# Performance work log

Hardware: AMD Instinct MI355X
Metric: run time of the kernel (lower is better)

Reference implementation:

```python
import jax, jax.numpy as jnp
import numpy as np

N_NODES = 50000
N_EDGES = 800000
IN_FEATS = 96
H_FEATS = 256
N_HOPS = 3
N_NIE = N_HOPS + 1  # hops 0..3
NDIM_FC = N_NIE * H_FEATS


def setup_inputs() -> dict:
    key = jax.random.key(0)
    ks = jax.random.split(key, 8)
    edge_index = jax.random.randint(ks[0], (2, N_EDGES), 0, N_NODES, dtype=jnp.int64)
    features = jax.random.normal(ks[1], (N_NODES, IN_FEATS), dtype=jnp.float32)
    # per-hop MLP params: Linear(in_feats, h_feats) for each of n_nie hops
    s_in = 1.0 / np.sqrt(IN_FEATS)
    Ws = jax.random.uniform(ks[2], (N_NIE, IN_FEATS, H_FEATS), jnp.float32, -s_in, s_in)
    bs = jax.random.uniform(ks[3], (N_NIE, H_FEATS), jnp.float32, -s_in, s_in)
    # fusion: Linear(ndim_fc, h_feats)
    s_fc = 1.0 / np.sqrt(NDIM_FC)
    Wf = jax.random.uniform(ks[4], (NDIM_FC, H_FEATS), jnp.float32, -s_fc, s_fc)
    bf = jax.random.uniform(ks[5], (H_FEATS,), jnp.float32, -s_fc, s_fc)
    return {"edge_index": edge_index, "features": features, "Ws": Ws, "bs": bs, "Wf": Wf, "bf": bf}


def _build_norm_adj(edge_index):
    """set_diag (remove existing diag, add unit self-loops) + symmetric D^-1/2 A D^-1/2.
    Returns (rows, cols, edge_w) COO of the normalized adjacency."""
    row, col = edge_index[0].astype(jnp.int32), edge_index[1].astype(jnp.int32)
    loop = jnp.arange(N_NODES, dtype=jnp.int32)
    rows = jnp.concatenate([row, loop])
    cols = jnp.concatenate([col, loop])
    # zero out any pre-existing diagonal entries, self-loops get weight 1 (set_diag semantics)
    w = jnp.concatenate([(row != col).astype(jnp.float32), jnp.ones((N_NODES,), jnp.float32)])
    deg = jax.ops.segment_sum(w, rows, num_segments=N_NODES)
    dinv = jnp.where(deg > 0, jax.lax.rsqrt(deg), 0.0)
    edge_w = dinv[rows] * w * dinv[cols]
    return rows, cols, edge_w


def _spmm(rows, cols, edge_w, x):
    # out[r] = sum_e w_e * x[cols[e]] for edges with rows[e]==r
    return jax.ops.segment_sum(edge_w[:, None] * x[cols], rows, num_segments=N_NODES)


def reference(edge_index, features, Ws, bs, Wf, bf):
    rows, cols, edge_w = _build_norm_adj(edge_index)
    # row-normalize features (F.normalize dim=1)
    x = features / jnp.maximum(jnp.linalg.norm(features, axis=1, keepdims=True), 1e-12)
    nei_feats = [x]
    h = x
    for _ in range(N_HOPS):
        h = _spmm(rows, cols, edge_w, h)
        nei_feats.append(h)
    # per-hop MLP (dropout p=0 -> identity; norm=None -> identity) then ReLU
    ns = [jax.nn.relu(nei_feats[i] @ Ws[i] + bs[i]) for i in range(N_NIE)]
    cat = jnp.concatenate(ns, axis=1)  # [N, ndim_fc]
    out = jax.nn.relu(cat @ Wf + bf)   # [N, h_feats]
    return out
```

## Files before the change

kernel.cpp:

```cpp
#include <hip/hip_runtime.h>

#define N_NODES 50000
#define N_EDGES 800000
#define IN_F 96
#define H_F 256
#define N_NIE 4
#define SCAN_NB 196
#define BM 64
#define NBLK 782
#define LDA1 104

typedef float f32x4 __attribute__((ext_vector_type(4)));
typedef short s16x8 __attribute__((ext_vector_type(8)));
typedef unsigned short ushort;

__device__ __forceinline__ ushort bf16_rne(float f) {
    unsigned u = __float_as_uint(f);
    u += 0x7fffu + ((u >> 16) & 1u);
    return (ushort)(u >> 16);
}
__device__ __forceinline__ float bf16_f(ushort h) {
    return __uint_as_float(((unsigned)h) << 16);
}

__global__ __launch_bounds__(256) void k_count(const int* __restrict__ rows,
                                               const int* __restrict__ cols,
                                               int* __restrict__ cnt) {
    int i = blockIdx.x * 256 + threadIdx.x;
    if (i >= N_EDGES / 2) return;
    int2 r2 = ((const int2*)rows)[i];
    int2 c2 = ((const int2*)cols)[i];
    if (r2.x != c2.x) atomicAdd(&cnt[r2.x], 1);
    if (r2.y != c2.y) atomicAdd(&cnt[r2.y], 1);
}

__global__ __launch_bounds__(256) void k_scan1(const int* __restrict__ cnt,
                                               int* __restrict__ rowptr,
                                               int* __restrict__ bsum) {
    __shared__ int s[256];
    int t = threadIdx.x, e = blockIdx.x * 256 + t;
    int v = (e < N_NODES) ? cnt[e] : 0;
    s[t] = v;
    __syncthreads();
    #pragma unroll
    for (int off = 1; off < 256; off <<= 1) {
        int nv = (t >= off) ? s[t - off] : 0;
        __syncthreads();
        s[t] += nv;
        __syncthreads();
    }
    if (e < N_NODES) rowptr[e] = s[t] - v;
    if (t == 255) bsum[blockIdx.x] = s[255];
}

__global__ __launch_bounds__(256) void k_scan2(int* __restrict__ bsum,
                                               int* __restrict__ boff,
                                               int* __restrict__ rowptr) {
    __shared__ int s[256];
    int t = threadIdx.x;
    int v = (t < SCAN_NB) ? bsum[t] : 0;
    s[t] = v;
    __syncthreads();
    #pragma unroll
    for (int off = 1; off < 256; off <<= 1) {
        int nv = (t >= off) ? s[t - off] : 0;
        __syncthreads();
        s[t] += nv;
        __syncthreads();
    }
    if (t < SCAN_NB) boff[t] = s[t] - v;
    if (t == 255) rowptr[N_NODES] = s[255];
}

__global__ __launch_bounds__(256) void k_scan3(const int* __restrict__ boff,
                                               const int* __restrict__ cnt,
                                               int* __restrict__ rowptr,
                                               int* __restrict__ cursor,
                                               float* __restrict__ dinv) {
    int e = blockIdx.x * 256 + threadIdx.x;
    if (e >= N_NODES) return;
    int r = rowptr[e] + boff[blockIdx.x];
    rowptr[e] = r;
    cursor[e] = r;
    dinv[e] = rsqrtf((float)cnt[e] + 1.0f);
}

__global__ __launch_bounds__(256) void k_scatter(const int* __restrict__ rows,
                                                 const int* __restrict__ cols,
                                                 const float* __restrict__ dinv,
                                                 int* __restrict__ cursor,
                                                 int2* __restrict__ cw) {
    int e = blockIdx.x * 256 + threadIdx.x;
    if (e >= N_EDGES) return;
    int r = rows[e], c = cols[e];
    if (r == c) return;
    int p = atomicAdd(&cursor[r], 1);
    long long v = ((long long)(unsigned)__float_as_int(dinv[c]) << 32) | (unsigned)c;
    __builtin_nontemporal_store(v, (long long*)&cw[p]);
}

__global__ __launch_bounds__(256) void k_wsplit_ws(const float* __restrict__ src,
                                                   ushort* __restrict__ dst) {
    int idx = blockIdx.x * 256 + threadIdx.x;
    if (idx >= N_NIE * IN_F * H_F) return;
    int hop = idx / (IN_F * H_F), rem = idx % (IN_F * H_F);
    int k = rem / H_F, n = rem % H_F;
    int c = n >> 6, wc = (n >> 5) & 1, b = (n >> 4) & 1, rsel = n & 15;
    int ks = k >> 5, kk = k & 31;
    int lane = (kk >> 3) * 16 + rsel, sel8 = kk & 7;
    int d = (((((hop * 4 + c) * 2 + wc) * 2 + b) * 3 + ks) * 64 + lane) * 8 + sel8;
    dst[d] = bf16_rne(src[idx]);
}

__global__ __launch_bounds__(256) void k_wsplit_wf(const float* __restrict__ src,
                                                   ushort* __restrict__ dst) {
    int idx = blockIdx.x * 256 + threadIdx.x;
    if (idx >= N_NIE * H_F * H_F) return;
    int hop = idx / (H_F * H_F), rem = idx % (H_F * H_F);
    int k = rem / H_F, n = rem % H_F;
    int kc = k >> 5, kk = k & 31;
    int w = n >> 5, rem2 = n & 31;
    int cf = rem2 >> 4, rsel = rem2 & 15;
    int lane = (kk >> 3) * 16 + rsel, sel8 = kk & 7;
    int d = ((((hop * 8 + kc) * 8 + w) * 2 + cf) * 64 + lane) * 8 + sel8;
    dst[d] = bf16_rne(src[idx]);
}

__global__ __launch_bounds__(256) void k_norm(const float* __restrict__ feat,
                                              ushort* __restrict__ x) {
    int wid = (blockIdx.x * 256 + threadIdx.x) >> 6;
    int lane = threadIdx.x & 63;
    if (wid >= N_NODES) return;
    const float* fr = feat + (size_t)wid * IN_F;
    float v0 = (lane < IN_F) ? fr[lane] : 0.0f;
    float v1 = (lane < IN_F - 64) ? fr[64 + lane] : 0.0f;
    float ss = v0 * v0 + v1 * v1;
    #pragma unroll
    for (int o = 32; o; o >>= 1) ss += __shfl_xor(ss, o, 64);
    float inv = 1.0f / fmaxf(sqrtf(ss), 1e-12f);
    ushort* xr = x + (size_t)wid * IN_F;
    if (lane < IN_F) xr[lane] = bf16_rne(v0 * inv);
    if (lane < IN_F - 64) xr[64 + lane] = bf16_rne(v1 * inv);
}

__global__ __launch_bounds__(256) void k_spmm_csr(const int* __restrict__ rowptr,
                                                  const int2* __restrict__ cw,
                                                  const float* __restrict__ dinv,
                                                  const ushort* __restrict__ x,
                                                  ushort* __restrict__ y) {
    int g = (blockIdx.x * 256 + threadIdx.x) >> 5;
    if (g >= N_NODES) return;
    int l = threadIdx.x & 31;
    float dr = dinv[g];
    const ushort* xg = x + (size_t)g * IN_F;
    float s0 = bf16_f(xg[l]), s1 = bf16_f(xg[l + 32]), s2 = bf16_f(xg[l + 64]);
    float a0 = 0.f, a1 = 0.f, a2 = 0.f;
    float b0 = 0.f, b1 = 0.f, b2 = 0.f;
    float c0 = 0.f, c1 = 0.f, c2 = 0.f;
    float d0 = 0.f, d1 = 0.f, d2 = 0.f;
    int k = rowptr[g], e = rowptr[g + 1];
    for (; k + 3 < e; k += 4) {
        int2 p0 = cw[k], p1 = cw[k + 1], p2 = cw[k + 2], p3 = cw[k + 3];
        const ushort* x0 = x + (size_t)p0.x * IN_F;
        const ushort* x1 = x + (size_t)p1.x * IN_F;
        const ushort* x2 = x + (size_t)p2.x * IN_F;
        const ushort* x3 = x + (size_t)p3.x * IN_F;
        float w0 = __int_as_float(p0.y), w1 = __int_as_float(p1.y);
        float w2 = __int_as_float(p2.y), w3 = __int_as_float(p3.y);
        a0 += bf16_f(x0[l]) * w0; a1 += bf16_f(x0[l + 32]) * w0; a2 += bf16_f(x0[l + 64]) * w0;
        b0 += bf16_f(x1[l]) * w1; b1 += bf16_f(x1[l + 32]) * w1; b2 += bf16_f(x1[l + 64]) * w1;
        c0 += bf16_f(x2[l]) * w2; c1 += bf16_f(x2[l + 32]) * w2; c2 += bf16_f(x2[l + 64]) * w2;
        d0 += bf16_f(x3[l]) * w3; d1 += bf16_f(x3[l + 32]) * w3; d2 += bf16_f(x3[l + 64]) * w3;
    }
    for (; k < e; ++k) {
        int2 p0 = cw[k];
        float w0 = __int_as_float(p0.y);
        const ushort* x0 = x + (size_t)p0.x * IN_F;
        a0 += bf16_f(x0[l]) * w0; a1 += bf16_f(x0[l + 32]) * w0; a2 += bf16_f(x0[l + 64]) * w0;
    }
    ushort* yr = y + (size_t)g * IN_F;
    yr[l]      = bf16_rne(dr * ((a0 + b0) + (c0 + d0) + dr * s0));
    yr[l + 32] = bf16_rne(dr * ((a1 + b1) + (c1 + d1) + dr * s1));
    yr[l + 64] = bf16_rne(dr * ((a2 + b2) + (c2 + d2) + dr * s2));
}

__global__ __launch_bounds__(512, 4) void k_mega(const ushort* __restrict__ h0,
                                                 const ushort* __restrict__ h1,
                                                 const ushort* __restrict__ h2,
                                                 const ushort* __restrict__ h3,
                                                 const ushort* __restrict__ Ws2,
                                                 const float* __restrict__ bs,
                                                 const ushort* __restrict__ Wf2,
                                                 const float* __restrict__ bf,
                                                 float* __restrict__ out) {
    __shared__ ushort SM[23040];
    ushort* nsH = SM;
    ushort* Ah  = SM + 16384;
    float* T = (float*)SM;

    int m0 = blockIdx.x * BM;
    int tid = threadIdx.x;
    int lane = tid & 63, w = tid >> 6;
    int rsel = lane & 15, g = lane >> 4, ksel = g * 8;
    int crow = g * 4, ccol = rsel;
    int rw0 = (w & 3) * 16;
    int wc = w >> 2;
    int cwb = wc * 32;

    int sr0 = tid / 12, sj0 = tid - sr0 * 12;
    int f1 = tid + 512;
    int sr1 = f1 / 12, sj1 = f1 - sr1 * 12;

    f32x4 acc[4][2] = {};

    for (int hop = 0; hop < N_NIE; ++hop) {
        const ushort* A = (hop == 0) ? h0 : (hop == 1) ? h1 : (hop == 2) ? h2 : h3;
        const ushort* wsF = Ws2 + (size_t)hop * IN_F * H_F;
        const ushort* wfF = Wf2 + (size_t)hop * H_F * H_F;
        const float* bsi = bs + hop * H_F;

        {
            int gm = m0 + sr0;
            s16x8 v = {0, 0, 0, 0, 0, 0, 0, 0};
            if (gm < N_NODES) v = *(const s16x8*)&A[(size_t)gm * IN_F + sj0 * 8];
            *(s16x8*)&Ah[sr0 * LDA1 + sj0 * 8] = v;
            if (tid < 256) {
                int gm1 = m0 + sr1;
                s16x8 v1 = {0, 0, 0, 0, 0, 0, 0, 0};
                if (gm1 < N_NODES) v1 = *(const s16x8*)&A[(size_t)gm1 * IN_F + sj1 * 8];
                *(s16x8*)&Ah[sr1 * LDA1 + sj1 * 8] = v1;
            }
        }
        __syncthreads();
        #pragma unroll
        for (int c = 0; c < 4; ++c) {
            const ushort* bsrc = wsF + (size_t)((c * 2 + wc) * 2) * 3 * 64 * 8;
            f32x4 ac[2] = {};
            #pragma unroll
            for (int ks = 0; ks < 3; ++ks) {
                s16x8 ah = *(const s16x8*)&Ah[(rw0 + rsel) * LDA1 + ks * 32 + ksel];
                s16x8 b0 = *(const s16x8*)&bsrc[(size_t)(ks * 64 + lane) * 8];
                s16x8 b1 = *(const s16x8*)&bsrc[(size_t)((3 + ks) * 64 + lane) * 8];
                ac[0] = __builtin_amdgcn_mfma_f32_16x16x32_bf16(ah, b0, ac[0], 0, 0, 0);
                ac[1] = __builtin_amdgcn_mfma_f32_16x16x32_bf16(ah, b1, ac[1], 0, 0, 0);
            }
            #pragma unroll
            for (int cf = 0; cf < 2; ++cf) {
                int col = c * 64 + cwb + cf * 16 + ccol;
                float bb = bsi[col];
                #pragma unroll
                for (int ii = 0; ii < 4; ++ii) {
                    int row = rw0 + crow + ii;
                    nsH[row * 256 + (col ^ ((row & 7) << 3))] =
                        bf16_rne(fmaxf(ac[cf][ii] + bb, 0.f));
                }
            }
        }
        __syncthreads();
        #pragma unroll
        for (int kc = 0; kc < 8; ++kc) {
            int k0 = kc * 32 + ksel;
            s16x8 ah4[4];
            #pragma unroll
            for (int rf = 0; rf < 4; ++rf) {
                int row = rf * 16 + rsel;
                ah4[rf] = *(const s16x8*)&nsH[row * 256 + (k0 ^ ((row & 7) << 3))];
            }
            #pragma unroll
            for (int cf = 0; cf < 2; ++cf) {
                s16x8 bh = *(const s16x8*)&wfF[(size_t)(((kc * 8 + w) * 2 + cf) * 64 + lane) * 8];
                #pragma unroll
                for (int rf = 0; rf < 4; ++rf)
                    acc[rf][cf] = __builtin_amdgcn_mfma_f32_16x16x32_bf16(ah4[rf], bh, acc[rf][cf], 0, 0, 0);
            }
        }
        __syncthreads();
    }
    #pragma unroll
    for (int half = 0; half < 2; ++half) {
        __syncthreads();
        #pragma unroll
        for (int rf2 = 0; rf2 < 2; ++rf2) {
            int rf = half * 2 + rf2;
            #pragma unroll
            for (int cf = 0; cf < 2; ++cf) {
                int col = w * 32 + cf * 16 + ccol;
                #pragma unroll
                for (int ii = 0; ii < 4; ++ii)
                    T[(rf2 * 16 + crow + ii) * 260 + col] = acc[rf][cf][ii];
            }
        }
        __syncthreads();
        #pragma unroll
        for (int p = 0; p < 4; ++p) {
            int flat = tid + p * 512;
            int r = flat >> 6, jc = flat & 63;
            int gm = m0 + half * 32 + r;
            if (gm < N_NODES) {
                f32x4 v = *(f32x4*)&T[r * 260 + jc * 4];
                f32x4 bb = *(const f32x4*)&bf[jc * 4];
                f32x4 o;
                #pragma unroll
                for (int q = 0; q < 4; ++q) o[q] = fmaxf(v[q] + bb[q], 0.f);
                *(f32x4*)&out[(size_t)gm * H_F + jc * 4] = o;
            }
        }
    }
}

extern "C" void kernel_launch(void* const* d_in, const int* in_sizes, int n_in,
                              void* d_out, int out_size, void* d_ws, size_t ws_size,
                              hipStream_t stream) {
    const int* ei = (const int*)d_in[0];
    const int* rows = ei;
    const int* cols = ei + N_EDGES;
    const float* feat = (const float*)d_in[1];
    const float* Ws = (const float*)d_in[2];
    const float* bs = (const float*)d_in[3];
    const float* Wf = (const float*)d_in[4];
    const float* bf = (const float*)d_in[5];
    float* out = (float*)d_out;

    ushort* h0 = (ushort*)d_ws;
    ushort* h1 = h0 + (size_t)N_NODES * IN_F;
    ushort* h2 = h1 + (size_t)N_NODES * IN_F;
    ushort* h3 = h2 + (size_t)N_NODES * IN_F;
    ushort* Ws2 = h3 + (size_t)N_NODES * IN_F;
    ushort* Wf2 = Ws2 + N_NIE * IN_F * H_F;
    float* dinv = (float*)(Wf2 + N_NIE * H_F * H_F);
    int* rowptr = (int*)(dinv + N_NODES);
    int* bsum = rowptr + 50004;
    int* boff = bsum + 256;
    int2* cw = (int2*)(boff + 256);
    int* cnt = (int*)h1;
    int* cursor = cnt + N_NODES;

    hipMemsetAsync(cnt, 0, N_NODES * sizeof(int), stream);
    k_count<<<(N_EDGES / 2 + 255) / 256, 256, 0, stream>>>(rows, cols, cnt);
    k_scan1<<<SCAN_NB, 256, 0, stream>>>(cnt, rowptr, bsum);
    k_scan2<<<1, 256, 0, stream>>>(bsum, boff, rowptr);
    k_scan3<<<SCAN_NB, 256, 0, stream>>>(boff, cnt, rowptr, cursor, dinv);
    k_scatter<<<(N_EDGES + 255) / 256, 256, 0, stream>>>(rows, cols, dinv, cursor, cw);
    k_wsplit_ws<<<(N_NIE * IN_F * H_F + 255) / 256, 256, 0, stream>>>(Ws, Ws2);
    k_wsplit_wf<<<(N_NIE * H_F * H_F + 255) / 256, 256, 0, stream>>>(Wf, Wf2);
    k_norm<<<(N_NODES + 3) / 4, 256, 0, stream>>>(feat, h0);

    k_spmm_csr<<<(N_NODES * 32 + 255) / 256, 256, 0, stream>>>(rowptr, cw, dinv, h0, h1);
    k_spmm_csr<<<(N_NODES * 32 + 255) / 256, 256, 0, stream>>>(rowptr, cw, dinv, h1, h2);
    k_spmm_csr<<<(N_NODES * 32 + 255) / 256, 256, 0, stream>>>(rowptr, cw, dinv, h2, h3);
    k_mega<<<NBLK, 512, 0, stream>>>(h0, h1, h2, h3, Ws2, bs, Wf2, bf, out);
}
```

Baseline: 316.0 us.

## Vectorize SpMM gathers with 16-lane groups, drop packed weights, add MFMA priority hints

```diff
diff --git a/kernel.cpp b/kernel.cpp
--- a/kernel.cpp
+++ b/kernel.cpp
@@ -87,16 +87,14 @@
 
 __global__ __launch_bounds__(256) void k_scatter(const int* __restrict__ rows,
                                                  const int* __restrict__ cols,
-                                                 const float* __restrict__ dinv,
                                                  int* __restrict__ cursor,
-                                                 int2* __restrict__ cw) {
+                                                 int* __restrict__ cwi) {
     int e = blockIdx.x * 256 + threadIdx.x;
     if (e >= N_EDGES) return;
     int r = rows[e], c = cols[e];
     if (r == c) return;
     int p = atomicAdd(&cursor[r], 1);
-    long long v = ((long long)(unsigned)__float_as_int(dinv[c]) << 32) | (unsigned)c;
-    __builtin_nontemporal_store(v, (long long*)&cw[p]);
+    __builtin_nontemporal_store(c, &cwi[p]);
 }
 
 __global__ __launch_bounds__(256) void k_wsplit_ws(const float* __restrict__ src,
@@ -144,44 +142,50 @@
 }
 
 __global__ __launch_bounds__(256) void k_spmm_csr(const int* __restrict__ rowptr,
-                                                  const int2* __restrict__ cw,
+                                                  const int* __restrict__ cwi,
                                                   const float* __restrict__ dinv,
                                                   const ushort* __restrict__ x,
                                                   ushort* __restrict__ y) {
-    int g = (blockIdx.x * 256 + threadIdx.x) >> 5;
+    int g = (blockIdx.x * 256 + threadIdx.x) >> 4;
     if (g >= N_NODES) return;
-    int l = threadIdx.x & 31;
+    int l = threadIdx.x & 15;
+    bool act = l < 12;
     float dr = dinv[g];
-    const ushort* xg = x + (size_t)g * IN_F;
-    float s0 = bf16_f(xg[l]), s1 = bf16_f(xg[l + 32]), s2 = bf16_f(xg[l + 64]);
-    float a0 = 0.f, a1 = 0.f, a2 = 0.f;
-    float b0 = 0.f, b1 = 0.f, b2 = 0.f;
-    float c0 = 0.f, c1 = 0.f, c2 = 0.f;
-    float d0 = 0.f, d1 = 0.f, d2 = 0.f;
+    s16x8 sv = {0, 0, 0, 0, 0, 0, 0, 0};
+    if (act) sv = *(const s16x8*)&x[(size_t)g * IN_F + l * 8];
+    float a[8] = {}, b[8] = {};
     int k = rowptr[g], e = rowptr[g + 1];
     for (; k + 3 < e; k += 4) {
-        int2 p0 = cw[k], p1 = cw[k + 1], p2 = cw[k + 2], p3 = cw[k + 3];
-        const ushort* x0 = x + (size_t)p0.x * IN_F;
-        const ushort* x1 = x + (size_t)p1.x * IN_F;
-        const ushort* x2 = x + (size_t)p2.x * IN_F;
-        const ushort* x3 = x + (size_t)p3.x * IN_F;
-        float w0 = __int_as_float(p0.y), w1 = __int_as_float(p1.y);
-        float w2 = __int_as_float(p2.y), w3 = __int_as_float(p3.y);
-        a0 += bf16_f(x0[l]) * w0; a1 += bf16_f(x0[l + 32]) * w0; a2 += bf16_f(x0[l + 64]) * w0;
-        b0 += bf16_f(x1[l]) * w1; b1 += bf16_f(x1[l + 32]) * w1; b2 += bf16_f(x1[l + 64]) * w1;
-        c0 += bf16_f(x2[l]) * w2; c1 += bf16_f(x2[l + 32]) * w2; c2 += bf16_f(x2[l + 64]) * w2;
-        d0 += bf16_f(x3[l]) * w3; d1 += bf16_f(x3[l + 32]) * w3; d2 += bf16_f(x3[l + 64]) * w3;
+        int c0 = cwi[k], c1 = cwi[k + 1], c2 = cwi[k + 2], c3 = cwi[k + 3];
+        float w0 = dinv[c0], w1 = dinv[c1], w2 = dinv[c2], w3 = dinv[c3];
+        s16x8 v0 = {0, 0, 0, 0, 0, 0, 0, 0}, v1 = v0, v2 = v0, v3 = v0;
+        if (act) {
+            v0 = *(const s16x8*)&x[(size_t)c0 * IN_F + l * 8];
+            v1 = *(const s16x8*)&x[(size_t)c1 * IN_F + l * 8];
+            v2 = *(const s16x8*)&x[(size_t)c2 * IN_F + l * 8];
+            v3 = *(const s16x8*)&x[(size_t)c3 * IN_F + l * 8];
+        }
+        #pragma unroll
+        for (int q = 0; q < 8; ++q) {
+            a[q] += bf16_f((ushort)v0[q]) * w0 + bf16_f((ushort)v1[q]) * w1;
+            b[q] += bf16_f((ushort)v2[q]) * w2 + bf16_f((ushort)v3[q]) * w3;
+        }
     }
     for (; k < e; ++k) {
-        int2 p0 = cw[k];
-        float w0 = __int_as_float(p0.y);
-        const ushort* x0 = x + (size_t)p0.x * IN_F;
-        a0 += bf16_f(x0[l]) * w0; a1 += bf16_f(x0[l + 32]) * w0; a2 += bf16_f(x0[l + 64]) * w0;
-    }
-    ushort* yr = y + (size_t)g * IN_F;
-    yr[l]      = bf16_rne(dr * ((a0 + b0) + (c0 + d0) + dr * s0));
-    yr[l + 32] = bf16_rne(dr * ((a1 + b1) + (c1 + d1) + dr * s1));
-    yr[l + 64] = bf16_rne(dr * ((a2 + b2) + (c2 + d2) + dr * s2));
+        int c0 = cwi[k];
+        float w0 = dinv[c0];
+        s16x8 v0 = {0, 0, 0, 0, 0, 0, 0, 0};
+        if (act) v0 = *(const s16x8*)&x[(size_t)c0 * IN_F + l * 8];
+        #pragma unroll
+        for (int q = 0; q < 8; ++q) a[q] += bf16_f((ushort)v0[q]) * w0;
+    }
+    if (act) {
+        s16x8 o;
+        #pragma unroll
+        for (int q = 0; q < 8; ++q)
+            o[q] = (short)bf16_rne(dr * ((a[q] + b[q]) + dr * bf16_f((ushort)sv[q])));
+        *(s16x8*)&y[(size_t)g * IN_F + l * 8] = o;
+    }
 }
 
 __global__ __launch_bounds__(512, 4) void k_mega(const ushort* __restrict__ h0,
@@ -236,6 +240,7 @@
         for (int c = 0; c < 4; ++c) {
             const ushort* bsrc = wsF + (size_t)((c * 2 + wc) * 2) * 3 * 64 * 8;
             f32x4 ac[2] = {};
+            __builtin_amdgcn_s_setprio(1);
             #pragma unroll
             for (int ks = 0; ks < 3; ++ks) {
                 s16x8 ah = *(const s16x8*)&Ah[(rw0 + rsel) * LDA1 + ks * 32 + ksel];
@@ -244,6 +249,7 @@
                 ac[0] = __builtin_amdgcn_mfma_f32_16x16x32_bf16(ah, b0, ac[0], 0, 0, 0);
                 ac[1] = __builtin_amdgcn_mfma_f32_16x16x32_bf16(ah, b1, ac[1], 0, 0, 0);
             }
+            __builtin_amdgcn_s_setprio(0);
             #pragma unroll
             for (int cf = 0; cf < 2; ++cf) {
                 int col = c * 64 + cwb + cf * 16 + ccol;
@@ -266,6 +272,7 @@
                 int row = rf * 16 + rsel;
                 ah4[rf] = *(const s16x8*)&nsH[row * 256 + (k0 ^ ((row & 7) << 3))];
             }
+            __builtin_amdgcn_s_setprio(1);
             #pragma unroll
             for (int cf = 0; cf < 2; ++cf) {
                 s16x8 bh = *(const s16x8*)&wfF[(size_t)(((kc * 8 + w) * 2 + cf) * 64 + lane) * 8];
@@ -273,6 +280,7 @@
                 for (int rf = 0; rf < 4; ++rf)
                     acc[rf][cf] = __builtin_amdgcn_mfma_f32_16x16x32_bf16(ah4[rf], bh, acc[rf][cf], 0, 0, 0);
             }
+            __builtin_amdgcn_s_setprio(0);
         }
         __syncthreads();
     }
@@ -331,7 +339,7 @@
     int* rowptr = (int*)(dinv + N_NODES);
     int* bsum = rowptr + 50004;
     int* boff = bsum + 256;
-    int2* cw = (int2*)(boff + 256);
+    int* cwi = boff + 256;
     int* cnt = (int*)h1;
     int* cursor = cnt + N_NODES;
 
@@ -340,13 +348,13 @@
     k_scan1<<<SCAN_NB, 256, 0, stream>>>(cnt, rowptr, bsum);
     k_scan2<<<1, 256, 0, stream>>>(bsum, boff, rowptr);
     k_scan3<<<SCAN_NB, 256, 0, stream>>>(boff, cnt, rowptr, cursor, dinv);
-    k_scatter<<<(N_EDGES + 255) / 256, 256, 0, stream>>>(rows, cols, dinv, cursor, cw);
+    k_scatter<<<(N_EDGES + 255) / 256, 256, 0, stream>>>(rows, cols, cursor, cwi);
     k_wsplit_ws<<<(N_NIE * IN_F * H_F + 255) / 256, 256, 0, stream>>>(Ws, Ws2);
     k_wsplit_wf<<<(N_NIE * H_F * H_F + 255) / 256, 256, 0, stream>>>(Wf, Wf2);
     k_norm<<<(N_NODES + 3) / 4, 256, 0, stream>>>(feat, h0);
 
-    k_spmm_csr<<<(N_NODES * 32 + 255) / 256, 256, 0, stream>>>(rowptr, cw, dinv, h0, h1);
-    k_spmm_csr<<<(N_NODES * 32 + 255) / 256, 256, 0, stream>>>(rowptr, cw, dinv, h1, h2);
-    k_spmm_csr<<<(N_NODES * 32 + 255) / 256, 256, 0, stream>>>(rowptr, cw, dinv, h2, h3);
+    k_spmm_csr<<<(N_NODES * 16 + 255) / 256, 256, 0, stream>>>(rowptr, cwi, dinv, h0, h1);
+    k_spmm_csr<<<(N_NODES * 16 + 255) / 256, 256, 0, stream>>>(rowptr, cwi, dinv, h1, h2);
+    k_spmm_csr<<<(N_NODES * 16 + 255) / 256, 256, 0, stream>>>(rowptr, cwi, dinv, h2, h3);
     k_mega<<<NBLK, 512, 0, stream>>>(h0, h1, h2, h3, Ws2, bs, Wf2, bf, out);
 }
```

Measured after the change: 308.6 us. 2.3% less time.
